# Performance work log

Measured on AMD Instinct MI355X. Metric: run time of the kernel, lower is better.

Reference implementation:

```python
import jax, jax.numpy as jnp
import numpy as np

B, T, F, H, NH, L = 32, 512, 16, 64, 4, 2
HD = H // NH


def _ln(x, g, b, eps=1e-5):
    m = x.mean(-1, keepdims=True)
    v = ((x - m) ** 2).mean(-1, keepdims=True)
    return (x - m) / jnp.sqrt(v + eps) * g + b


def _glu(x, w, b):
    a, g = jnp.split(x @ w + b, 2, axis=-1)
    return a * jax.nn.sigmoid(g)


def _lstm_layer(x, w_ih, w_hh, b):
    # x: (B,T,H); PyTorch gate order i,f,g,o
    Bd = x.shape[0]

    def step(carry, xt):
        h, c = carry
        gates = xt @ w_ih + h @ w_hh + b
        i, f, g, o = jnp.split(gates, 4, axis=-1)
        c = jax.nn.sigmoid(f) * c + jax.nn.sigmoid(i) * jnp.tanh(g)
        h = jax.nn.sigmoid(o) * jnp.tanh(c)
        return (h, c), h

    z = jnp.zeros((Bd, H), x.dtype)
    _, hs = jax.lax.scan(step, (z, z), jnp.swapaxes(x, 0, 1))
    return jnp.swapaxes(hs, 0, 1)


def setup_inputs() -> dict:
    key = jax.random.key(0)
    specs = [
        ("x", (B, T, F), "n"),
        ("ip_w", (H,), "n"), ("ip_b", (H,), "n"),
        ("vsn_fc1_w", (F, H, H), "n"), ("vsn_fc1_b", (F, H), "n"),
        ("vsn_fc2_w", (F, H, 2 * H), "n"), ("vsn_fc2_b", (F, 2 * H), "n"),
        ("vsn_ln_g", (F, H), "1"), ("vsn_ln_b", (F, H), "0"),
        ("sel_fc1_w", (F * H, H), "n"), ("sel_fc1_b", (H,), "n"),
        ("sel_fc2_w", (H, 2 * F), "n"), ("sel_fc2_b", (2 * F,), "n"),
        ("sel_skip_w", (F * H, F), "n"), ("sel_skip_b", (F,), "n"),
        ("sel_ln_g", (F,), "1"), ("sel_ln_b", (F,), "0"),
        ("lstm_w_ih", (L, H, 4 * H), "n"), ("lstm_w_hh", (L, H, 4 * H), "n"), ("lstm_b", (L, 4 * H), "n"),
        ("plg_w", (H, 2 * H), "n"), ("plg_b", (2 * H,), "n"),
        ("pln_g", (H,), "1"), ("pln_b", (H,), "0"),
        ("qkv_w", (H, 3 * H), "n"), ("qkv_b", (3 * H,), "n"),
        ("ao_w", (H, H), "n"), ("ao_b", (H,), "n"),
        ("pag_w", (H, 2 * H), "n"), ("pag_b", (2 * H,), "n"),
        ("pan_g", (H,), "1"), ("pan_b", (H,), "0"),
        ("ff1_w", (H, 4 * H), "n"), ("ff1_b", (4 * H,), "n"),
        ("ff2_w", (4 * H, 2 * H), "n"), ("ff2_b", (2 * H,), "n"),
        ("ffln_g", (H,), "1"), ("ffln_b", (H,), "0"),
        ("fn_g", (H,), "1"), ("fn_b", (H,), "0"),
        ("out_w", (H, 1), "n"), ("out_b", (1,), "n"),
    ]
    keys = jax.random.split(key, len(specs))
    d = {}
    for (name, shp, kind), k in zip(specs, keys):
        if kind == "n":
            scale = 1.0 if name == "x" else 0.05
            d[name] = jax.random.normal(k, shp, jnp.float32) * scale
        elif kind == "1":
            d[name] = jnp.ones(shp, jnp.float32)
        else:
            d[name] = jnp.zeros(shp, jnp.float32)
    return d


def reference(x, ip_w, ip_b, vsn_fc1_w, vsn_fc1_b, vsn_fc2_w, vsn_fc2_b, vsn_ln_g, vsn_ln_b,
              sel_fc1_w, sel_fc1_b, sel_fc2_w, sel_fc2_b, sel_skip_w, sel_skip_b, sel_ln_g, sel_ln_b,
              lstm_w_ih, lstm_w_hh, lstm_b, plg_w, plg_b, pln_g, pln_b,
              qkv_w, qkv_b, ao_w, ao_b, pag_w, pag_b, pan_g, pan_b,
              ff1_w, ff1_b, ff2_w, ff2_b, ffln_g, ffln_b, fn_g, fn_b, out_w, out_b):
    Bd, Td, Fd = x.shape
    # input_proj: Linear(1,H) applied to each scalar feature -> (B,T,F,H)
    xp = x[..., None] * ip_w + ip_b
    # --- VSN (vectorized over B and T; torch loops over T and F) ---
    flat = xp.reshape(Bd, Td, Fd * H)
    h = jax.nn.elu(flat @ sel_fc1_w + sel_fc1_b)
    a, g = jnp.split(h @ sel_fc2_w + sel_fc2_b, 2, axis=-1)
    sel = _ln(a * jax.nn.sigmoid(g) + (flat @ sel_skip_w + sel_skip_b), sel_ln_g, sel_ln_b)
    w = jax.nn.softmax(sel, axis=-1)  # (B,T,F)
    h = jax.nn.elu(jnp.einsum('btfi,fio->btfo', xp, vsn_fc1_w) + vsn_fc1_b)
    a, g = jnp.split(jnp.einsum('btfi,fio->btfo', h, vsn_fc2_w) + vsn_fc2_b, 2, axis=-1)
    proc = _ln(a * jax.nn.sigmoid(g) + xp, vsn_ln_g, vsn_ln_b)  # (B,T,F,H)
    vsn_out = jnp.einsum('btf,btfh->bth', w, proc)
    # --- 2-layer LSTM encoder (dropout inactive in eval) ---
    seq = vsn_out
    for l in range(L):
        seq = _lstm_layer(seq, lstm_w_ih[l], lstm_w_hh[l], lstm_b[l])
    lo = _ln(_glu(seq, plg_w, plg_b) + vsn_out, pln_g, pln_b)
    # --- self-attention ---
    q, k, v = jnp.split(lo @ qkv_w + qkv_b, 3, axis=-1)
    q = q.reshape(Bd, Td, NH, HD)
    k = k.reshape(Bd, Td, NH, HD)
    v = v.reshape(Bd, Td, NH, HD)
    sc = jnp.einsum('bqhd,bkhd->bhqk', q, k) / jnp.sqrt(jnp.float32(HD))
    att = jnp.einsum('bhqk,bkhd->bqhd', jax.nn.softmax(sc, axis=-1), v).reshape(Bd, Td, H)
    att = att @ ao_w + ao_b
    at = _ln(_glu(att, pag_w, pag_b) + lo, pan_g, pan_b)
    # --- FF GRN + final norm ---
    h = jax.nn.elu(at @ ff1_w + ff1_b)
    a, g = jnp.split(h @ ff2_w + ff2_b, 2, axis=-1)
    ff = _ln(a * jax.nn.sigmoid(g) + at, ffln_g, ffln_b)
    ff = _ln(ff + at, fn_g, fn_b)
    return ff[:, -1, :] @ out_w + out_b  # (B, forecast_horizon)
```

## Files before the change

### kernel.cpp

```cpp
#include <hip/hip_runtime.h>
#include <math.h>


__device__ __forceinline__ float sigf(float x){
    return 1.f / (1.f + __expf(-x));
}
__device__ __forceinline__ float tanhf_(float x){
    float xc = fminf(fmaxf(x, -15.f), 15.f);
    float e = __expf(-2.f * xc);
    return (1.f - e) / (1.f + e);
}
__device__ __forceinline__ float eluf(float x){
    return x > 0.f ? x : (__expf(x) - 1.f);
}
__device__ __forceinline__ float wsum64(float v){
    #pragma unroll
    for (int o = 1; o < 64; o <<= 1) v += __shfl_xor(v, o, 64);
    return v;
}
__device__ __forceinline__ float wmax64(float v){
    #pragma unroll
    for (int o = 1; o < 64; o <<= 1) v = fmaxf(v, __shfl_xor(v, o, 64));
    return v;
}

#define BARRIER_LGKM() do {                                    \
    asm volatile("s_waitcnt lgkmcnt(0)" ::: "memory");         \
    __builtin_amdgcn_s_barrier();                              \
} while(0)

__global__ __launch_bounds__(512) void tft_vsn_kernel(
    const float* __restrict__ x,
    const float* __restrict__ ip_w, const float* __restrict__ ip_b,
    const float* __restrict__ vfc1w, const float* __restrict__ vfc1b,
    const float* __restrict__ vfc2w, const float* __restrict__ vfc2b,
    const float* __restrict__ vlng, const float* __restrict__ vlnb,
    const float* __restrict__ sfc1w, const float* __restrict__ sfc1b,
    const float* __restrict__ sfc2w, const float* __restrict__ sfc2b,
    const float* __restrict__ sskw, const float* __restrict__ sskb,
    const float* __restrict__ slng, const float* __restrict__ slnb,
    float* __restrict__ vsn_out)
{
    __shared__ __align__(16) float s_x[64*16];
    __shared__ __align__(16) float s_ipw[64];
    __shared__ __align__(16) float s_ipb[64];
    __shared__ __align__(16) float s_xp[64*65];
    __shared__ __align__(16) float s_W1[64*64];
    __shared__ __align__(16) float s_W2[64*128];
    __shared__ __align__(16) float s_Wsk[64*16];
    __shared__ __align__(16) float s_h[64*65];
    __shared__ __align__(16) float s_sel2[64*32];
    __shared__ __align__(16) float s_wsm[64*16];
    __shared__ __align__(16) float s_lng[64];
    __shared__ __align__(16) float s_lnb[64];
    __shared__ __align__(16) float s_b1[64];
    __shared__ __align__(16) float s_b2[128];

    const int tid  = threadIdx.x;
    const int pos0 = blockIdx.x * 64;
    const int m    = tid >> 3;
    const int g8   = tid & 7;
    const int j0   = g8 * 8;

    if (tid < 256) ((float4*)s_x)[tid] = *(const float4*)(x + pos0*16 + tid*4);
    if (tid < 64) { s_ipw[tid] = ip_w[tid]; s_ipb[tid] = ip_b[tid]; }
    __syncthreads();

    float accS[8];
    #pragma unroll
    for (int i = 0; i < 8; i++) accS[i] = 0.f;
    float accK0 = 0.f, accK1 = 0.f;

    for (int f = 0; f < 16; f++){
        {
            float xb = s_x[m*16 + f];
            #pragma unroll
            for (int i = 0; i < 8; i++)
                s_xp[m*65 + j0 + i] = xb * s_ipw[j0+i] + s_ipb[j0+i];
        }
        #pragma unroll
        for (int i = 0; i < 2; i++)
            ((float4*)s_W1)[tid + i*512] = *(const float4*)(sfc1w + f*4096 + (tid + i*512)*4);
        if (tid < 256) ((float4*)s_Wsk)[tid] = *(const float4*)(sskw + f*1024 + tid*4);
        __syncthreads();
        #pragma unroll 8
        for (int k = 0; k < 64; k++){
            float xv = s_xp[m*65 + k];
            const float4* wr = (const float4*)(s_W1 + k*64 + j0);
            float4 w0 = wr[0], w1 = wr[1];
            accS[0] += xv*w0.x; accS[1] += xv*w0.y; accS[2] += xv*w0.z; accS[3] += xv*w0.w;
            accS[4] += xv*w1.x; accS[5] += xv*w1.y; accS[6] += xv*w1.z; accS[7] += xv*w1.w;
            float2 wk = *(const float2*)(s_Wsk + k*16 + g8*2);
            accK0 += xv*wk.x; accK1 += xv*wk.y;
        }
        __syncthreads();
    }

    #pragma unroll
    for (int i = 0; i < 8; i++)
        s_h[m*65 + j0 + i] = eluf(accS[i] + sfc1b[j0+i]);
    ((float4*)s_W1)[tid] = *(const float4*)(sfc2w + tid*4);
    __syncthreads();

    {
        const int jj = g8 * 4;
        float a0 = 0.f, a1 = 0.f, a2 = 0.f, a3 = 0.f;
        #pragma unroll 8
        for (int k = 0; k < 64; k++){
            float hv = s_h[m*65 + k];
            float4 w = *(const float4*)(s_W1 + k*32 + jj);
            a0 += hv*w.x; a1 += hv*w.y; a2 += hv*w.z; a3 += hv*w.w;
        }
        s_sel2[m*32 + jj+0] = a0 + sfc2b[jj+0];
        s_sel2[m*32 + jj+1] = a1 + sfc2b[jj+1];
        s_sel2[m*32 + jj+2] = a2 + sfc2b[jj+2];
        s_sel2[m*32 + jj+3] = a3 + sfc2b[jj+3];
    }
    __syncthreads();

    {
        const int f0 = g8 * 2;
        float a0 = s_sel2[m*32 + f0],   g0 = s_sel2[m*32 + 16 + f0];
        float a1 = s_sel2[m*32 + f0+1], g1 = s_sel2[m*32 + 16 + f0+1];
        float pre0 = a0*sigf(g0) + accK0 + sskb[f0];
        float pre1 = a1*sigf(g1) + accK1 + sskb[f0+1];
        float sum = pre0 + pre1;
        sum += __shfl_xor(sum,1,8); sum += __shfl_xor(sum,2,8); sum += __shfl_xor(sum,4,8);
        float mean = sum * 0.0625f;
        float d0 = pre0 - mean, d1 = pre1 - mean;
        float vv = d0*d0 + d1*d1;
        vv += __shfl_xor(vv,1,8); vv += __shfl_xor(vv,2,8); vv += __shfl_xor(vv,4,8);
        float rstd = rsqrtf(vv * 0.0625f + 1e-5f);
        float sv0 = d0*rstd*slng[f0]   + slnb[f0];
        float sv1 = d1*rstd*slng[f0+1] + slnb[f0+1];
        float mx = fmaxf(sv0, sv1);
        mx = fmaxf(mx, __shfl_xor(mx,1,8));
        mx = fmaxf(mx, __shfl_xor(mx,2,8));
        mx = fmaxf(mx, __shfl_xor(mx,4,8));
        float e0 = __expf(sv0 - mx), e1 = __expf(sv1 - mx);
        float es = e0 + e1;
        es += __shfl_xor(es,1,8); es += __shfl_xor(es,2,8); es += __shfl_xor(es,4,8);
        float inv = 1.f / es;
        s_wsm[m*16 + f0]   = e0 * inv;
        s_wsm[m*16 + f0+1] = e1 * inv;
    }
    __syncthreads();

    float accV[8];
    #pragma unroll
    for (int i = 0; i < 8; i++) accV[i] = 0.f;

    for (int f = 0; f < 16; f++){
        {
            float xb = s_x[m*16 + f];
            #pragma unroll
            for (int i = 0; i < 8; i++)
                s_xp[m*65 + j0 + i] = xb * s_ipw[j0+i] + s_ipb[j0+i];
        }
        #pragma unroll
        for (int i = 0; i < 2; i++)
            ((float4*)s_W1)[tid + i*512] = *(const float4*)(vfc1w + f*4096 + (tid + i*512)*4);
        #pragma unroll
        for (int i = 0; i < 4; i++)
            ((float4*)s_W2)[tid + i*512] = *(const float4*)(vfc2w + f*8192 + (tid + i*512)*4);
        if (tid < 16)       ((float4*)s_b1)[tid]     = *(const float4*)(vfc1b + f*64  + tid*4);
        else if (tid < 48)  ((float4*)s_b2)[tid-16]  = *(const float4*)(vfc2b + f*128 + (tid-16)*4);
        else if (tid < 64)  ((float4*)s_lng)[tid-48] = *(const float4*)(vlng  + f*64  + (tid-48)*4);
        else if (tid < 80)  ((float4*)s_lnb)[tid-64] = *(const float4*)(vlnb  + f*64  + (tid-64)*4);
        __syncthreads();

        float ah[8];
        #pragma unroll
        for (int i = 0; i < 8; i++) ah[i] = 0.f;
        #pragma unroll 8
        for (int k = 0; k < 64; k++){
            float xv = s_xp[m*65 + k];
            const float4* wr = (const float4*)(s_W1 + k*64 + j0);
            float4 w0 = wr[0], w1 = wr[1];
            ah[0] += xv*w0.x; ah[1] += xv*w0.y; ah[2] += xv*w0.z; ah[3] += xv*w0.w;
            ah[4] += xv*w1.x; ah[5] += xv*w1.y; ah[6] += xv*w1.z; ah[7] += xv*w1.w;
        }
        #pragma unroll
        for (int i = 0; i < 8; i++)
            s_h[m*65 + j0 + i] = eluf(ah[i] + s_b1[j0+i]);
        __syncthreads();

        float aa[8], ag[8];
        #pragma unroll
        for (int i = 0; i < 8; i++){ aa[i] = 0.f; ag[i] = 0.f; }
        #pragma unroll 4
        for (int k = 0; k < 64; k++){
            float hv = s_h[m*65 + k];
            const float4* war = (const float4*)(s_W2 + k*128 + j0);
            const float4* wgr = (const float4*)(s_W2 + k*128 + 64 + j0);
            float4 wa0 = war[0], wa1 = war[1];
            float4 wg0 = wgr[0], wg1 = wgr[1];
            aa[0] += hv*wa0.x; aa[1] += hv*wa0.y; aa[2] += hv*wa0.z; aa[3] += hv*wa0.w;
            aa[4] += hv*wa1.x; aa[5] += hv*wa1.y; aa[6] += hv*wa1.z; aa[7] += hv*wa1.w;
            ag[0] += hv*wg0.x; ag[1] += hv*wg0.y; ag[2] += hv*wg0.z; ag[3] += hv*wg0.w;
            ag[4] += hv*wg1.x; ag[5] += hv*wg1.y; ag[6] += hv*wg1.z; ag[7] += hv*wg1.w;
        }
        float pre[8];
        float lsum = 0.f;
        #pragma unroll
        for (int i = 0; i < 8; i++){
            float av = aa[i] + s_b2[j0+i];
            float gv = ag[i] + s_b2[64 + j0+i];
            pre[i] = av * sigf(gv) + s_xp[m*65 + j0 + i];
            lsum += pre[i];
        }
        lsum += __shfl_xor(lsum,1,8); lsum += __shfl_xor(lsum,2,8); lsum += __shfl_xor(lsum,4,8);
        float mean = lsum * 0.015625f;
        float lvar = 0.f;
        #pragma unroll
        for (int i = 0; i < 8; i++){ float d = pre[i] - mean; lvar += d*d; }
        lvar += __shfl_xor(lvar,1,8); lvar += __shfl_xor(lvar,2,8); lvar += __shfl_xor(lvar,4,8);
        float rstd = rsqrtf(lvar * 0.015625f + 1e-5f);
        float wf = s_wsm[m*16 + f];
        #pragma unroll
        for (int i = 0; i < 8; i++)
            accV[i] += wf * ((pre[i] - mean) * rstd * s_lng[j0+i] + s_lnb[j0+i]);
        __syncthreads();
    }

    float4 o0 = make_float4(accV[0], accV[1], accV[2], accV[3]);
    float4 o1 = make_float4(accV[4], accV[5], accV[6], accV[7]);
    *(float4*)(vsn_out + (pos0 + m)*64 + j0)     = o0;
    *(float4*)(vsn_out + (pos0 + m)*64 + j0 + 4) = o1;
}

__global__ __launch_bounds__(256) void tft_xgates_kernel(
    const float* __restrict__ vsn, const float* __restrict__ w_ih,
    const float* __restrict__ bias, float* __restrict__ gpre)
{
    __shared__ __align__(16) float s_w[64*256];
    __shared__ __align__(16) float s_vT[64*20];
    __shared__ __align__(16) float s_b[256];
    const int tid  = threadIdx.x;
    const int pos0 = blockIdx.x * 16;

    #pragma unroll
    for (int i = 0; i < 16; i++)
        ((float4*)s_w)[tid + i*256] = *(const float4*)(w_ih + (tid + i*256)*4);
    s_b[tid] = bias[tid];
    {
        int mm = tid >> 4;
        int k0 = (tid & 15) * 4;
        float4 v = *(const float4*)(vsn + (pos0 + mm)*64 + k0);
        s_vT[(k0+0)*20 + mm] = v.x;
        s_vT[(k0+1)*20 + mm] = v.y;
        s_vT[(k0+2)*20 + mm] = v.z;
        s_vT[(k0+3)*20 + mm] = v.w;
    }
    __syncthreads();

    float acc[16];
    #pragma unroll
    for (int i = 0; i < 16; i++) acc[i] = 0.f;
    #pragma unroll 8
    for (int k = 0; k < 64; k++){
        float wv = s_w[k*256 + tid];
        const float4* vr = (const float4*)(s_vT + k*20);
        float4 v0 = vr[0], v1 = vr[1], v2 = vr[2], v3 = vr[3];
        acc[0]  += wv*v0.x; acc[1]  += wv*v0.y; acc[2]  += wv*v0.z; acc[3]  += wv*v0.w;
        acc[4]  += wv*v1.x; acc[5]  += wv*v1.y; acc[6]  += wv*v1.z; acc[7]  += wv*v1.w;
        acc[8]  += wv*v2.x; acc[9]  += wv*v2.y; acc[10] += wv*v2.z; acc[11] += wv*v2.w;
        acc[12] += wv*v3.x; acc[13] += wv*v3.y; acc[14] += wv*v3.z; acc[15] += wv*v3.w;
    }
    float bv = s_b[tid];
    #pragma unroll
    for (int i = 0; i < 16; i++)
        gpre[(pos0 + i)*256 + tid] = acc[i] + bv;
}

#define LDW4(P, i) make_float4((P)[(4*(i)+0)*256], (P)[(4*(i)+1)*256], \
                               (P)[(4*(i)+2)*256], (P)[(4*(i)+3)*256])

#define LSTM_CH(c) {                                                        \
    float4 h1c = h1b[c];                                                    \
    a10 += h1c.x*W1_##c.x; a11 += h1c.y*W1_##c.y;                           \
    a12 += h1c.z*W1_##c.z; a13 += h1c.w*W1_##c.w;                           \
    a20 += h1c.x*WX_##c.x; a21 += h1c.y*WX_##c.y;                           \
    a22 += h1c.z*WX_##c.z; a23 += h1c.w*WX_##c.w;                           \
    float4 h2c = h2b[c];                                                    \
    a20 += h2c.x*WH_##c.x; a21 += h2c.y*WH_##c.y;                           \
    a22 += h2c.z*WH_##c.z; a23 += h2c.w*WH_##c.w;                           \
}

__global__ __launch_bounds__(512, 1) void tft_lstm_kernel(
    const float* __restrict__ w_ih, const float* __restrict__ w_hh,
    const float* __restrict__ bias, const float* __restrict__ gpre,
    float* __restrict__ seq)
{
    __shared__ __align__(16) float s_h1[64];
    __shared__ __align__(16) float s_h2[64];
    __shared__ __align__(16) float s_g1h[512];
    __shared__ __align__(16) float s_g2h[512];
    __shared__ __align__(16) float s_gp[256];

    const int tid  = threadIdx.x;
    const int b    = blockIdx.x;
    const int g    = tid & 255;
    const int half = tid >> 8;
    const int koff = half * 32;

    const float* p1 = w_hh + koff*256 + g;
    const float* px = w_ih + 16384 + koff*256 + g;
    const float* ph = w_hh + 16384 + koff*256 + g;

    float4 W1_0 = LDW4(p1,0), W1_1 = LDW4(p1,1), W1_2 = LDW4(p1,2), W1_3 = LDW4(p1,3);
    float4 W1_4 = LDW4(p1,4), W1_5 = LDW4(p1,5), W1_6 = LDW4(p1,6), W1_7 = LDW4(p1,7);
    float4 WX_0 = LDW4(px,0), WX_1 = LDW4(px,1), WX_2 = LDW4(px,2), WX_3 = LDW4(px,3);
    float4 WX_4 = LDW4(px,4), WX_5 = LDW4(px,5), WX_6 = LDW4(px,6), WX_7 = LDW4(px,7);
    float4 WH_0 = LDW4(ph,0), WH_1 = LDW4(ph,1), WH_2 = LDW4(ph,2), WH_3 = LDW4(ph,3);
    float4 WH_4 = LDW4(ph,4), WH_5 = LDW4(ph,5), WH_6 = LDW4(ph,6), WH_7 = LDW4(ph,7);

    const float b2 = (half == 0) ? bias[256 + g] : 0.f;

    if (tid < 64) s_h1[tid] = 0.f;
    else if (tid < 128) s_h2[tid - 64] = 0.f;

    const float* gpb = gpre + (size_t)b * 512 * 256 + g;
    float gp_w = 0.f, gp_l = 0.f;
    if (half == 0){
        s_gp[g] = gpb[0];
        gp_w    = gpb[256];
        gp_l    = gpb[512];
    }
    float c1 = 0.f, c2 = 0.f;
    __syncthreads();

    const float4* h1b = (const float4*)s_h1 + half*8;
    const float4* h2b = (const float4*)s_h2 + half*8;
    float* seqb = seq + (size_t)b * 512 * 64;

    for (int n = 0; n <= 512; ++n){
        float a10 = (half == 0) ? s_gp[g] : 0.f;
        float a11 = 0.f, a12 = 0.f, a13 = 0.f;
        float a20 = b2, a21 = 0.f, a22 = 0.f, a23 = 0.f;
        LSTM_CH(0) LSTM_CH(1) LSTM_CH(2) LSTM_CH(3)
        LSTM_CH(4) LSTM_CH(5) LSTM_CH(6) LSTM_CH(7)
        float gp_n = 0.f;
        if (half == 0 && n + 3 < 512) gp_n = gpb[(n + 3) * 256];
        s_g1h[half*256 + g] = (a10 + a11) + (a12 + a13);
        s_g2h[half*256 + g] = (a20 + a21) + (a22 + a23);
        BARRIER_LGKM();

        if (tid < 64 && n < 512){
            float gi = s_g1h[tid]     + s_g1h[256+tid];
            float gf = s_g1h[64+tid]  + s_g1h[320+tid];
            float gg = s_g1h[128+tid] + s_g1h[384+tid];
            float go = s_g1h[192+tid] + s_g1h[448+tid];
            c1 = sigf(gf)*c1 + sigf(gi)*tanhf_(gg);
            s_h1[tid] = sigf(go)*tanhf_(c1);
        } else if (tid >= 64 && tid < 128 && n >= 1){
            int j = tid - 64;
            float gi = s_g2h[j]     + s_g2h[256+j];
            float gf = s_g2h[64+j]  + s_g2h[320+j];
            float gg = s_g2h[128+j] + s_g2h[384+j];
            float go = s_g2h[192+j] + s_g2h[448+j];
            c2 = sigf(gf)*c2 + sigf(gi)*tanhf_(gg);
            float h2v = sigf(go)*tanhf_(c2);
            s_h2[j] = h2v;
            seqb[(size_t)(n - 1)*64 + j] = h2v;
        }
        if (half == 0 && n + 1 < 512) s_gp[g] = gp_w;
        gp_w = gp_l; gp_l = gp_n;
        BARRIER_LGKM();
    }
}

__global__ __launch_bounds__(256) void tft_lokv_kernel(
    const float* __restrict__ seq, const float* __restrict__ vsn,
    const float* __restrict__ plgw, const float* __restrict__ plgb,
    const float* __restrict__ png,  const float* __restrict__ pnb,
    const float* __restrict__ qkvw, const float* __restrict__ qkvb,
    float* __restrict__ kbuf, float* __restrict__ vbuf,
    float* __restrict__ qlast, float* __restrict__ lolast)
{
    __shared__ __align__(16) float s_pw[64*128];
    __shared__ __align__(16) float s_qw[64*192];
    __shared__ __align__(16) float s_pb[128];
    __shared__ __align__(16) float s_png[64];
    __shared__ __align__(16) float s_pnb[64];
    __shared__ __align__(16) float s_qb[192];
    __shared__ __align__(16) float s_row[4][64];
    __shared__ __align__(16) float s_lo[4][64];

    const int tid  = threadIdx.x;
    const int lane = tid & 63;
    const int wid  = tid >> 6;

    #pragma unroll
    for (int i = 0; i < 8; i++)
        ((float4*)s_pw)[tid + i*256] = *(const float4*)(plgw + (tid + i*256)*4);
    #pragma unroll
    for (int i = 0; i < 12; i++)
        ((float4*)s_qw)[tid + i*256] = *(const float4*)(qkvw + (tid + i*256)*4);
    if (tid < 128) s_pb[tid] = plgb[tid];
    if (tid < 64){ s_png[tid] = png[tid]; s_pnb[tid] = pnb[tid]; }
    if (tid < 192) s_qb[tid] = qkvb[tid];
    __syncthreads();

    for (int it = 0; it < 16; it++){
        int mpos = blockIdx.x*64 + wid*16 + it;
        int b = mpos >> 9, t = mpos & 511;
        float sv = seq[mpos*64 + lane];
        float vs = vsn[mpos*64 + lane];
        s_row[wid][lane] = sv;
        __syncthreads();
        float a = s_pb[lane], g = s_pb[64 + lane];
        #pragma unroll 8
        for (int k = 0; k < 64; k++){
            float rv = s_row[wid][k];
            a += rv * s_pw[k*128 + lane];
            g += rv * s_pw[k*128 + 64 + lane];
        }
        float pre = a * sigf(g) + vs;
        float mean = wsum64(pre) * 0.015625f;
        float d = pre - mean;
        float vv = wsum64(d*d) * 0.015625f;
        float lo = d * rsqrtf(vv + 1e-5f) * s_png[lane] + s_pnb[lane];
        s_lo[wid][lane] = lo;
        __syncthreads();
        float ka = s_qb[64 + lane], va = s_qb[128 + lane];
        #pragma unroll 8
        for (int k = 0; k < 64; k++){
            float lv = s_lo[wid][k];
            ka += lv * s_qw[k*192 + 64 + lane];
            va += lv * s_qw[k*192 + 128 + lane];
        }
        int h = lane >> 4, dd = lane & 15;
        kbuf[((b*4 + h)*512 + t)*16 + dd] = ka;
        vbuf[((b*4 + h)*512 + t)*16 + dd] = va;
        if (t == 511){
            float qa = s_qb[lane];
            #pragma unroll 8
            for (int k = 0; k < 64; k++)
                qa += s_lo[wid][k] * s_qw[k*192 + lane];
            qlast[b*64 + lane] = qa;
            lolast[b*64 + lane] = lo;
        }
    }
}

__global__ __launch_bounds__(256) void tft_head_kernel(
    const float* __restrict__ kbuf, const float* __restrict__ vbuf,
    const float* __restrict__ qlast, const float* __restrict__ lolast,
    const float* __restrict__ aow,  const float* __restrict__ aob,
    const float* __restrict__ pagw, const float* __restrict__ pagb,
    const float* __restrict__ pang, const float* __restrict__ panb,
    const float* __restrict__ ff1w, const float* __restrict__ ff1b,
    const float* __restrict__ ff2w, const float* __restrict__ ff2b,
    const float* __restrict__ fflng, const float* __restrict__ fflnb,
    const float* __restrict__ fng,  const float* __restrict__ fnb,
    const float* __restrict__ outw, const float* __restrict__ outb,
    float* __restrict__ out)
{
    __shared__ __align__(16) float s_q[64];
    __shared__ __align__(16) float s_lo[64];
    __shared__ __align__(16) float s_sc[4*512];
    __shared__ __align__(16) float s_part[4][64];
    __shared__ __align__(16) float s_a[64];
    __shared__ __align__(16) float s_a2[64];
    __shared__ __align__(16) float s_z[128];
    __shared__ __align__(16) float s_at[64];
    __shared__ __align__(16) float s_f1[256];

    const int tid = threadIdx.x;
    const int b   = blockIdx.x;
    if (tid < 64){ s_q[tid] = qlast[b*64 + tid]; s_lo[tid] = lolast[b*64 + tid]; }
    __syncthreads();

    for (int idx = tid; idx < 2048; idx += 256){
        int h = idx >> 9, t = idx & 511;
        const float4* kr = (const float4*)(kbuf + ((b*4 + h)*512 + t)*16);
        const float4* qr = (const float4*)(s_q + h*16);
        float4 k0 = kr[0], k1 = kr[1], k2 = kr[2], k3 = kr[3];
        float4 q0 = qr[0], q1 = qr[1], q2 = qr[2], q3 = qr[3];
        float d = q0.x*k0.x + q0.y*k0.y + q0.z*k0.z + q0.w*k0.w
                + q1.x*k1.x + q1.y*k1.y + q1.z*k1.z + q1.w*k1.w
                + q2.x*k2.x + q2.y*k2.y + q2.z*k2.z + q2.w*k2.w
                + q3.x*k3.x + q3.y*k3.y + q3.z*k3.z + q3.w*k3.w;
        s_sc[idx] = d * 0.25f;
    }
    __syncthreads();
    {
        int h = tid >> 6, lane = tid & 63;
        float v[8];
        float mx = -1e30f;
        #pragma unroll
        for (int j = 0; j < 8; j++){ v[j] = s_sc[h*512 + lane + j*64]; mx = fmaxf(mx, v[j]); }
        mx = wmax64(mx);
        float sum = 0.f;
        #pragma unroll
        for (int j = 0; j < 8; j++){ v[j] = __expf(v[j] - mx); sum += v[j]; }
        sum = wsum64(sum);
        float inv = 1.f / sum;
        #pragma unroll
        for (int j = 0; j < 8; j++) s_sc[h*512 + lane + j*64] = v[j] * inv;
    }
    __syncthreads();
    {
        int j = tid & 63, part = tid >> 6;
        int h = j >> 4, dd = j & 15;
        float pa = 0.f;
        for (int t = part*128; t < (part+1)*128; t++)
            pa += s_sc[h*512 + t] * vbuf[((b*4 + h)*512 + t)*16 + dd];
        s_part[part][j] = pa;
    }
    __syncthreads();
    if (tid < 64) s_a[tid] = s_part[0][tid] + s_part[1][tid] + s_part[2][tid] + s_part[3][tid];
    __syncthreads();
    if (tid < 64){
        float o = aob[tid];
        #pragma unroll 8
        for (int k = 0; k < 64; k++) o += s_a[k] * aow[k*64 + tid];
        s_a2[tid] = o;
    }
    __syncthreads();
    if (tid < 128){
        float z = pagb[tid];
        #pragma unroll 8
        for (int k = 0; k < 64; k++) z += s_a2[k] * pagw[k*128 + tid];
        s_z[tid] = z;
    }
    __syncthreads();
    if (tid < 64){
        float pre = s_z[tid] * sigf(s_z[64 + tid]) + s_lo[tid];
        float mean = wsum64(pre) * 0.015625f;
        float d = pre - mean;
        float vv = wsum64(d*d) * 0.015625f;
        s_at[tid] = d * rsqrtf(vv + 1e-5f) * pang[tid] + panb[tid];
    }
    __syncthreads();
    {
        float hv = ff1b[tid];
        #pragma unroll 8
        for (int k = 0; k < 64; k++) hv += s_at[k] * ff1w[k*256 + tid];
        s_f1[tid] = eluf(hv);
    }
    __syncthreads();
    if (tid < 128){
        float z = ff2b[tid];
        #pragma unroll 8
        for (int k = 0; k < 256; k++) z += s_f1[k] * ff2w[k*128 + tid];
        s_z[tid] = z;
    }
    __syncthreads();
    if (tid < 64){
        float pre = s_z[tid] * sigf(s_z[64 + tid]) + s_at[tid];
        float mean = wsum64(pre) * 0.015625f;
        float d = pre - mean;
        float vv = wsum64(d*d) * 0.015625f;
        float ffv = d * rsqrtf(vv + 1e-5f) * fflng[tid] + fflnb[tid];
        float pre2 = ffv + s_at[tid];
        float mean2 = wsum64(pre2) * 0.015625f;
        float d2 = pre2 - mean2;
        float v2 = wsum64(d2*d2) * 0.015625f;
        float f2 = d2 * rsqrtf(v2 + 1e-5f) * fng[tid] + fnb[tid];
        float p = wsum64(f2 * outw[tid]);
        if (tid == 0) out[b] = p + outb[0];
    }
}

extern "C" void kernel_launch(void* const* d_in, const int* in_sizes, int n_in,
                              void* d_out, int out_size, void* d_ws, size_t ws_size,
                              hipStream_t stream)
{
    const float* x     = (const float*)d_in[0];
    const float* ip_w  = (const float*)d_in[1];
    const float* ip_b  = (const float*)d_in[2];
    const float* vfc1w = (const float*)d_in[3];
    const float* vfc1b = (const float*)d_in[4];
    const float* vfc2w = (const float*)d_in[5];
    const float* vfc2b = (const float*)d_in[6];
    const float* vlng  = (const float*)d_in[7];
    const float* vlnb  = (const float*)d_in[8];
    const float* sfc1w = (const float*)d_in[9];
    const float* sfc1b = (const float*)d_in[10];
    const float* sfc2w = (const float*)d_in[11];
    const float* sfc2b = (const float*)d_in[12];
    const float* sskw  = (const float*)d_in[13];
    const float* sskb  = (const float*)d_in[14];
    const float* slng  = (const float*)d_in[15];
    const float* slnb  = (const float*)d_in[16];
    const float* lwih  = (const float*)d_in[17];
    const float* lwhh  = (const float*)d_in[18];
    const float* lb    = (const float*)d_in[19];
    const float* plgw  = (const float*)d_in[20];
    const float* plgb  = (const float*)d_in[21];
    const float* plng  = (const float*)d_in[22];
    const float* plnb  = (const float*)d_in[23];
    const float* qkvw  = (const float*)d_in[24];
    const float* qkvb  = (const float*)d_in[25];
    const float* aow   = (const float*)d_in[26];
    const float* aob   = (const float*)d_in[27];
    const float* pagw  = (const float*)d_in[28];
    const float* pagb  = (const float*)d_in[29];
    const float* pang  = (const float*)d_in[30];
    const float* panb  = (const float*)d_in[31];
    const float* ff1w  = (const float*)d_in[32];
    const float* ff1b  = (const float*)d_in[33];
    const float* ff2w  = (const float*)d_in[34];
    const float* ff2b  = (const float*)d_in[35];
    const float* fflng = (const float*)d_in[36];
    const float* fflnb = (const float*)d_in[37];
    const float* fng   = (const float*)d_in[38];
    const float* fnb   = (const float*)d_in[39];
    const float* outw  = (const float*)d_in[40];
    const float* outb  = (const float*)d_in[41];

    float* ws      = (float*)d_ws;
    float* vsn_out = ws;
    float* seq     = ws + 1048576;
    float* gpre    = ws + 2*1048576;
    float* kbuf    = ws + 6*1048576;
    float* vbuf    = ws + 7*1048576;
    float* qlast   = ws + 8*1048576;
    float* lolast  = qlast + 2048;
    float* outp    = (float*)d_out;

    tft_vsn_kernel<<<256, 512, 0, stream>>>(x, ip_w, ip_b, vfc1w, vfc1b, vfc2w, vfc2b,
                                            vlng, vlnb, sfc1w, sfc1b, sfc2w, sfc2b,
                                            sskw, sskb, slng, slnb, vsn_out);
    tft_xgates_kernel<<<1024, 256, 0, stream>>>(vsn_out, lwih, lb, gpre);
    tft_lstm_kernel<<<32, 512, 0, stream>>>(lwih, lwhh, lb, gpre, seq);
    tft_lokv_kernel<<<256, 256, 0, stream>>>(seq, vsn_out, plgw, plgb, plng, plnb,
                                             qkvw, qkvb, kbuf, vbuf, qlast, lolast);
    tft_head_kernel<<<32, 256, 0, stream>>>(kbuf, vbuf, qlast, lolast, aow, aob,
                                            pagw, pagb, pang, panb, ff1w, ff1b,
                                            ff2w, ff2b, fflng, fflnb, fng, fnb,
                                            outw, outb, outp);
}
```

Before: 765.4 us.

## Use fp16 packed dot products and shuffle-based gate exchange in LSTM recurrence

The recurrent LSTM kernel now keeps its weights as packed fp16 pairs in registers and computes the recurrent matvecs with fdot2. Each thread owns gate pairs, so the four gates of a hidden unit are combined with cross-lane shuffles rather than a shared-memory partial-sum round trip. Hidden state is double-buffered in LDS as packed halves, which drops one barrier per timestep, and the block grows to 768 threads so each layer gets its own waves. This targets the serial per-step latency of the recurrence, at the cost of fp16 rounding of the weights and hidden state that may compound over 512 steps.

Result: slower. 796.8 us (+4.1%).

```diff
diff --git a/kernel.cpp b/kernel.cpp
--- a/kernel.cpp
+++ b/kernel.cpp
@@ -1,6 +1,11 @@
 #include <hip/hip_runtime.h>
 #include <math.h>
 
+
+typedef __fp16 half2_t __attribute__((ext_vector_type(2)));
+union h2u_t { unsigned u; half2_t h; };
+__device__ __forceinline__ half2_t u2h(unsigned u){ h2u_t x; x.u = u; return x.h; }
+__device__ __forceinline__ unsigned h2u(half2_t h){ h2u_t x; x.h = h; return x.u; }
 
 __device__ __forceinline__ float sigf(float x){
     return 1.f / (1.f + __expf(-x));
@@ -273,99 +278,141 @@
         gpre[(pos0 + i)*256 + tid] = acc[i] + bv;
 }
 
-#define LDW4(P, i) make_float4((P)[(4*(i)+0)*256], (P)[(4*(i)+1)*256], \
-                               (P)[(4*(i)+2)*256], (P)[(4*(i)+3)*256])
-
-#define LSTM_CH(c) {                                                        \
-    float4 h1c = h1b[c];                                                    \
-    a10 += h1c.x*W1_##c.x; a11 += h1c.y*W1_##c.y;                           \
-    a12 += h1c.z*W1_##c.z; a13 += h1c.w*W1_##c.w;                           \
-    a20 += h1c.x*WX_##c.x; a21 += h1c.y*WX_##c.y;                           \
-    a22 += h1c.z*WX_##c.z; a23 += h1c.w*WX_##c.w;                           \
-    float4 h2c = h2b[c];                                                    \
-    a20 += h2c.x*WH_##c.x; a21 += h2c.y*WH_##c.y;                           \
-    a22 += h2c.z*WH_##c.z; a23 += h2c.w*WH_##c.w;                           \
-}
-
-__global__ __launch_bounds__(512, 1) void tft_lstm_kernel(
+#define PKWU(P, r) h2u(__builtin_amdgcn_cvt_pkrtz((P)[(2*(r))*256], (P)[(2*(r)+1)*256]))
+#define PINU(V) asm volatile("" : "+v"(V))
+
+#define DOTC(c, wa0, wa1, wb0, wb1, A, B) {                                 \
+    uint2 qq = hp[c];                                                       \
+    half2_t x0 = u2h(qq.x), x1 = u2h(qq.y);                                 \
+    A = __builtin_amdgcn_fdot2(u2h(wa0), x0, A, false);                     \
+    A = __builtin_amdgcn_fdot2(u2h(wa1), x1, A, false);                     \
+    B = __builtin_amdgcn_fdot2(u2h(wb0), x0, B, false);                     \
+    B = __builtin_amdgcn_fdot2(u2h(wb1), x1, B, false); }
+
+__global__ __launch_bounds__(768, 1) void tft_lstm_kernel(
     const float* __restrict__ w_ih, const float* __restrict__ w_hh,
     const float* __restrict__ bias, const float* __restrict__ gpre,
     float* __restrict__ seq)
 {
-    __shared__ __align__(16) float s_h1[64];
-    __shared__ __align__(16) float s_h2[64];
-    __shared__ __align__(16) float s_g1h[512];
-    __shared__ __align__(16) float s_g2h[512];
-    __shared__ __align__(16) float s_gp[256];
+    __shared__ __align__(16) unsigned s_h1[2][32];
+    __shared__ __align__(16) unsigned s_h2[2][32];
 
     const int tid  = threadIdx.x;
     const int b    = blockIdx.x;
-    const int g    = tid & 255;
-    const int half = tid >> 8;
-    const int koff = half * 32;
-
-    const float* p1 = w_hh + koff*256 + g;
-    const float* px = w_ih + 16384 + koff*256 + g;
-    const float* ph = w_hh + 16384 + koff*256 + g;
-
-    float4 W1_0 = LDW4(p1,0), W1_1 = LDW4(p1,1), W1_2 = LDW4(p1,2), W1_3 = LDW4(p1,3);
-    float4 W1_4 = LDW4(p1,4), W1_5 = LDW4(p1,5), W1_6 = LDW4(p1,6), W1_7 = LDW4(p1,7);
-    float4 WX_0 = LDW4(px,0), WX_1 = LDW4(px,1), WX_2 = LDW4(px,2), WX_3 = LDW4(px,3);
-    float4 WX_4 = LDW4(px,4), WX_5 = LDW4(px,5), WX_6 = LDW4(px,6), WX_7 = LDW4(px,7);
-    float4 WH_0 = LDW4(ph,0), WH_1 = LDW4(ph,1), WH_2 = LDW4(ph,2), WH_3 = LDW4(ph,3);
-    float4 WH_4 = LDW4(ph,4), WH_5 = LDW4(ph,5), WH_6 = LDW4(ph,6), WH_7 = LDW4(ph,7);
-
-    const float b2 = (half == 0) ? bias[256 + g] : 0.f;
-
-    if (tid < 64) s_h1[tid] = 0.f;
-    else if (tid < 128) s_h2[tid - 64] = 0.f;
-
-    const float* gpb = gpre + (size_t)b * 512 * 256 + g;
-    float gp_w = 0.f, gp_l = 0.f;
-    if (half == 0){
-        s_gp[g] = gpb[0];
-        gp_w    = gpb[256];
-        gp_l    = gpb[512];
-    }
-    float c1 = 0.f, c2 = 0.f;
-    __syncthreads();
-
-    const float4* h1b = (const float4*)s_h1 + half*8;
-    const float4* h2b = (const float4*)s_h2 + half*8;
-    float* seqb = seq + (size_t)b * 512 * 64;
+    const int lane = tid & 63;
+    const int wid  = tid >> 6;
+    const bool isL2 = (wid >= 4);
+    const int gpair = lane >> 5;
+
+    int j, seg;
+    if (!isL2){ j = (wid << 4) | (lane & 15); seg = (lane >> 4) & 1; }
+    else      { j = ((wid - 4) << 3) | (lane & 7); seg = (lane >> 3) & 3; }
+
+    const int g0 = (gpair ? 64 : 0) + j;
+    const int g1 = (gpair ? 192 : 128) + j;
+
+    const float* mat;
+    int row0;
+    if (!isL2){ mat = w_hh; row0 = seg * 32; }
+    else { mat = (seg < 2) ? (w_ih + 16384) : (w_hh + 16384); row0 = (seg & 1) * 32; }
+    const float* pA = mat + row0 * 256 + g0;
+    const float* pB = mat + row0 * 256 + g1;
+
+    unsigned WA_0 = PKWU(pA,0),  WA_1 = PKWU(pA,1),  WA_2 = PKWU(pA,2),  WA_3 = PKWU(pA,3);
+    unsigned WA_4 = PKWU(pA,4),  WA_5 = PKWU(pA,5),  WA_6 = PKWU(pA,6),  WA_7 = PKWU(pA,7);
+    unsigned WA_8 = PKWU(pA,8),  WA_9 = PKWU(pA,9),  WA_10= PKWU(pA,10), WA_11= PKWU(pA,11);
+    unsigned WA_12= PKWU(pA,12), WA_13= PKWU(pA,13), WA_14= PKWU(pA,14), WA_15= PKWU(pA,15);
+    unsigned WB_0 = PKWU(pB,0),  WB_1 = PKWU(pB,1),  WB_2 = PKWU(pB,2),  WB_3 = PKWU(pB,3);
+    unsigned WB_4 = PKWU(pB,4),  WB_5 = PKWU(pB,5),  WB_6 = PKWU(pB,6),  WB_7 = PKWU(pB,7);
+    unsigned WB_8 = PKWU(pB,8),  WB_9 = PKWU(pB,9),  WB_10= PKWU(pB,10), WB_11= PKWU(pB,11);
+    unsigned WB_12= PKWU(pB,12), WB_13= PKWU(pB,13), WB_14= PKWU(pB,14), WB_15= PKWU(pB,15);
+    PINU(WA_0);  PINU(WA_1);  PINU(WA_2);  PINU(WA_3);
+    PINU(WA_4);  PINU(WA_5);  PINU(WA_6);  PINU(WA_7);
+    PINU(WA_8);  PINU(WA_9);  PINU(WA_10); PINU(WA_11);
+    PINU(WA_12); PINU(WA_13); PINU(WA_14); PINU(WA_15);
+    PINU(WB_0);  PINU(WB_1);  PINU(WB_2);  PINU(WB_3);
+    PINU(WB_4);  PINU(WB_5);  PINU(WB_6);  PINU(WB_7);
+    PINU(WB_8);  PINU(WB_9);  PINU(WB_10); PINU(WB_11);
+    PINU(WB_12); PINU(WB_13); PINU(WB_14); PINU(WB_15);
+
+    float bA = 0.f, bB = 0.f;
+    if (isL2 && seg == 0){ bA = bias[256 + g0]; bB = bias[256 + g1]; }
+
+    const bool gpl = (!isL2 && seg == 0);
+    const float* gA = gpre + (size_t)b * 131072 + g0;
+    const float* gB = gpre + (size_t)b * 131072 + g1;
+    float qA0=0.f,qA1=0.f,qA2=0.f, qB0=0.f,qB1=0.f,qB2=0.f;
+    if (gpl){
+        qA0 = gA[0];   qB0 = gB[0];
+        qA1 = gA[256]; qB1 = gB[256];
+        qA2 = gA[512]; qB2 = gB[512];
+    }
+
+    if (tid < 32){ s_h1[0][tid] = 0u; s_h1[1][tid] = 0u; }
+    else if (tid < 64){ s_h2[0][tid-32] = 0u; s_h2[1][tid-32] = 0u; }
+    float c_ = 0.f;
+    __syncthreads();
+
+    float* seqb = seq + (size_t)b * 32768;
+    const int hword = (isL2 ? (seg & 1) : seg) * 16;
 
     for (int n = 0; n <= 512; ++n){
-        float a10 = (half == 0) ? s_gp[g] : 0.f;
-        float a11 = 0.f, a12 = 0.f, a13 = 0.f;
-        float a20 = b2, a21 = 0.f, a22 = 0.f, a23 = 0.f;
-        LSTM_CH(0) LSTM_CH(1) LSTM_CH(2) LSTM_CH(3)
-        LSTM_CH(4) LSTM_CH(5) LSTM_CH(6) LSTM_CH(7)
-        float gp_n = 0.f;
-        if (half == 0 && n + 3 < 512) gp_n = gpb[(n + 3) * 256];
-        s_g1h[half*256 + g] = (a10 + a11) + (a12 + a13);
-        s_g2h[half*256 + g] = (a20 + a21) + (a22 + a23);
-        BARRIER_LGKM();
-
-        if (tid < 64 && n < 512){
-            float gi = s_g1h[tid]     + s_g1h[256+tid];
-            float gf = s_g1h[64+tid]  + s_g1h[320+tid];
-            float gg = s_g1h[128+tid] + s_g1h[384+tid];
-            float go = s_g1h[192+tid] + s_g1h[448+tid];
-            c1 = sigf(gf)*c1 + sigf(gi)*tanhf_(gg);
-            s_h1[tid] = sigf(go)*tanhf_(c1);
-        } else if (tid >= 64 && tid < 128 && n >= 1){
-            int j = tid - 64;
-            float gi = s_g2h[j]     + s_g2h[256+j];
-            float gf = s_g2h[64+j]  + s_g2h[320+j];
-            float gg = s_g2h[128+j] + s_g2h[384+j];
-            float go = s_g2h[192+j] + s_g2h[448+j];
-            c2 = sigf(gf)*c2 + sigf(gi)*tanhf_(gg);
-            float h2v = sigf(go)*tanhf_(c2);
-            s_h2[j] = h2v;
-            seqb[(size_t)(n - 1)*64 + j] = h2v;
-        }
-        if (half == 0 && n + 1 < 512) s_gp[g] = gp_w;
-        gp_w = gp_l; gp_l = gp_n;
+        const int cur = n & 1, prv = cur ^ 1;
+        const unsigned* hrd;
+        if (!isL2)          hrd = &s_h1[prv][hword];
+        else if (seg < 2)   hrd = &s_h1[prv][hword];
+        else                hrd = &s_h2[prv][hword];
+        const uint2* hp = (const uint2*)hrd;
+
+        float a0  = isL2 ? bA : (seg ? 0.f : qA0);
+        float a1  = isL2 ? bB : (seg ? 0.f : qB0);
+        float a0x = 0.f, a1x = 0.f;
+        DOTC(0, WA_0,  WA_1,  WB_0,  WB_1,  a0,  a1)
+        DOTC(1, WA_2,  WA_3,  WB_2,  WB_3,  a0x, a1x)
+        DOTC(2, WA_4,  WA_5,  WB_4,  WB_5,  a0,  a1)
+        DOTC(3, WA_6,  WA_7,  WB_6,  WB_7,  a0x, a1x)
+        DOTC(4, WA_8,  WA_9,  WB_8,  WB_9,  a0,  a1)
+        DOTC(5, WA_10, WA_11, WB_10, WB_11, a0x, a1x)
+        DOTC(6, WA_12, WA_13, WB_12, WB_13, a0,  a1)
+        DOTC(7, WA_14, WA_15, WB_14, WB_15, a0x, a1x)
+        float A = a0 + a0x;
+        float B = a1 + a1x;
+        if (isL2){
+            A += __shfl_xor(A, 8, 64);
+            B += __shfl_xor(B, 8, 64);
+        }
+        A += __shfl_xor(A, 16, 64);
+        B += __shfl_xor(B, 16, 64);
+        float oA = __shfl_xor(A, 32, 64);
+        float oB = __shfl_xor(B, 32, 64);
+        float gi = gpair ? oA : A;
+        float gf = gpair ? A  : oA;
+        float gg = gpair ? oB : B;
+        float go = gpair ? B  : oB;
+
+        if (gpl){
+            qA0 = qA1; qA1 = qA2; qB0 = qB1; qB1 = qB2;
+            if (n + 3 < 512){ qA2 = gA[(n+3)*256]; qB2 = gB[(n+3)*256]; }
+        }
+
+        if (!isL2){
+            if (n < 512){
+                c_ = sigf(gf)*c_ + sigf(gi)*tanhf_(gg);
+                float hv = sigf(go)*tanhf_(c_);
+                float hn = __shfl_xor(hv, 1, 64);
+                if ((lane & 48) == 0 && (j & 1) == 0)
+                    s_h1[cur][j >> 1] = h2u(__builtin_amdgcn_cvt_pkrtz(hv, hn));
+            }
+        } else if (n >= 1){
+            c_ = sigf(gf)*c_ + sigf(gi)*tanhf_(gg);
+            float hv = sigf(go)*tanhf_(c_);
+            float hn = __shfl_xor(hv, 1, 64);
+            if ((lane & 56) == 0){
+                if ((j & 1) == 0)
+                    s_h2[cur][j >> 1] = h2u(__builtin_amdgcn_cvt_pkrtz(hv, hn));
+                seqb[(n - 1)*64 + j] = hv;
+            }
+        }
         BARRIER_LGKM();
     }
 }
@@ -625,7 +672,7 @@
                                             vlng, vlnb, sfc1w, sfc1b, sfc2w, sfc2b,
                                             sskw, sskb, slng, slnb, vsn_out);
     tft_xgates_kernel<<<1024, 256, 0, stream>>>(vsn_out, lwih, lb, gpre);
-    tft_lstm_kernel<<<32, 512, 0, stream>>>(lwih, lwhh, lb, gpre, seq);
+    tft_lstm_kernel<<<32, 768, 0, stream>>>(lwih, lwhh, lb, gpre, seq);
     tft_lokv_kernel<<<256, 256, 0, stream>>>(seq, vsn_out, plgw, plgb, plng, plnb,
                                              qkvw, qkvb, kbuf, vbuf, qlast, lolast);
     tft_head_kernel<<<32, 256, 0, stream>>>(kbuf, vbuf, qlast, lolast, aow, aob,
```
